# Optimization experiments

Hardware: AMD Instinct MI355X
Metric: run time of the kernel (lower is better)

## Reference

```python
import jax, jax.numpy as jnp
import numpy as np

B, T, F, H = 256, 100, 256, 512
EPS = 1e-9


def _uni(k, shape, fan):
    s = 1.0 / np.sqrt(fan)
    return jax.random.uniform(k, shape, jnp.float32, -s, s)


def setup_inputs() -> dict:
    key = jax.random.key(0)
    ks = jax.random.split(key, 20)
    values = jax.random.normal(ks[0], (B, T, F), jnp.float32)
    masks = (jax.random.uniform(ks[1], (B, T, F)) > 0.2).astype(jnp.float32)
    deltas = jax.random.uniform(ks[2], (B, T, F), jnp.float32) * 5.0
    return {
        "values": values, "masks": masks, "deltas": deltas,
        # TemporalDecay h: W [H,F], stdv=1/sqrt(H)
        "W_td_h": _uni(ks[3], (H, F), H), "b_td_h": _uni(ks[4], (H,), H),
        # TemporalDecay x (diag): W [F,F], stdv=1/sqrt(F)
        "W_td_x": _uni(ks[5], (F, F), F), "b_td_x": _uni(ks[6], (F,), F),
        # hist_reg Linear(H->F): stdv=1/sqrt(H)
        "W_hist": _uni(ks[7], (F, H), H), "b_hist": _uni(ks[8], (F,), H),
        "W_feat": _uni(ks[9], (F, F), F), "b_feat": _uni(ks[10], (F,), F),
        # combining_weight Linear(2F->F): stdv=1/sqrt(2F)
        "W_comb": _uni(ks[11], (F, 2 * F), 2 * F), "b_comb": _uni(ks[12], (F,), 2 * F),
        # LSTMCell(2F -> H): stdv=1/sqrt(H)
        "W_ih": _uni(ks[13], (4 * H, 2 * F), H), "W_hh": _uni(ks[14], (4 * H, H), H),
        "b_ih": _uni(ks[15], (4 * H,), H), "b_hh": _uni(ks[16], (4 * H,), H),
    }


def _mae(pred, target, mask):
    return jnp.sum(jnp.abs(pred - target) * mask) / (jnp.sum(mask) + EPS)


def reference(values, masks, deltas, W_td_h, b_td_h, W_td_x, b_td_x,
              W_hist, b_hist, W_feat, b_feat, W_comb, b_comb,
              W_ih, W_hh, b_ih, b_hh):
    diag_td_x = jnp.diagonal(W_td_x)               # F.linear(d, W*eye) == d * diag(W)
    Wf_masked = W_feat * (1.0 - jnp.eye(F, dtype=W_feat.dtype))

    def step(carry, xs):
        h, c, loss = carry
        x, m, d = xs                               # [B,F] each
        gamma_h = jnp.exp(-jax.nn.relu(d @ W_td_h.T + b_td_h))   # [B,H]
        gamma_x = jnp.exp(-jax.nn.relu(d * diag_td_x + b_td_x))  # [B,F]
        h = h * gamma_h
        x_h = h @ W_hist.T + b_hist
        loss = loss + _mae(x_h, x, m)
        x_c = m * x + (1.0 - m) * x_h
        z_h = jax.nn.relu(x_c @ Wf_masked.T + b_feat)
        loss = loss + _mae(z_h, x, m)
        alpha = jax.nn.sigmoid(jnp.concatenate([gamma_x, m], axis=1) @ W_comb.T + b_comb)
        c_h = alpha * z_h + (1.0 - alpha) * x_h
        loss = loss + _mae(c_h, x, m)
        c_c = m * x + (1.0 - m) * c_h
        inp = jnp.concatenate([c_c, m], axis=1)    # [B,2F]
        gates = inp @ W_ih.T + b_ih + h @ W_hh.T + b_hh
        i_g, f_g, g_g, o_g = jnp.split(gates, 4, axis=1)
        c = jax.nn.sigmoid(f_g) * c + jax.nn.sigmoid(i_g) * jnp.tanh(g_g)
        h = jax.nn.sigmoid(o_g) * jnp.tanh(c)
        return (h, c, loss), c_h

    h0 = jnp.zeros((values.shape[0], H), values.dtype)
    c0 = jnp.zeros((values.shape[0], H), values.dtype)
    xs = (jnp.swapaxes(values, 0, 1), jnp.swapaxes(masks, 0, 1), jnp.swapaxes(deltas, 0, 1))
    (h, c, loss), ests = jax.lax.scan(step, (h0, c0, jnp.float32(0.0)), xs)
    estimations = jnp.swapaxes(ests, 0, 1)         # [B,T,F]
    imputed = masks * values + (1.0 - masks) * estimations
    recon_loss = loss / (T * 3)
    return imputed, h, recon_loss
```

## Files before the change

### kernel.cpp

```cpp
#include <hip/hip_runtime.h>
#include <math.h>


#define T_ 100

typedef unsigned short ushortT;
typedef __attribute__((ext_vector_type(8))) short short8;
typedef __attribute__((ext_vector_type(4))) float f32x4;

#define OB_HD0    1048576u
#define OB_HD1    1310720u
#define OB_XCB    1835008u
#define OB_CCB    1966080u
#define OB_NUM2   2097152u
#define OB_DEN    2122752u
#define OB_CNT    2123264u
#define OB_BIASP  2123776u
#define OB_BA     2131968u
#define OB_BB     2394112u
#define OB_BC     2525184u
#define OB_MT     6719488u
#define OB_GH     19826688u
#define OB_AL     46041088u
#define OB_FLG1   59148288u
#define OB_FLG2   59152384u

__device__ __forceinline__ float sigm(float x) { return 1.0f / (1.0f + expf(-x)); }

__device__ __forceinline__ ushortT f2bf(float f) {
    union { float f; unsigned u; } v; v.f = f;
    unsigned r = v.u + 0x7fffu + ((v.u >> 16) & 1u);
    return (ushortT)(r >> 16);
}
__device__ __forceinline__ float bf2f(ushortT h) {
    union { unsigned u; float f; } v; v.u = ((unsigned)h) << 16; return v.f;
}

__device__ __forceinline__ void st_bf16_wt(ushortT* p, ushortT v) {
    asm volatile("global_store_short %0, %1, off sc0 sc1" :: "v"(p), "v"((unsigned)v) : "memory");
}
__device__ __forceinline__ void st_f32_wt(float* p, float v) {
    asm volatile("global_store_dword %0, %1, off sc0 sc1" :: "v"(p), "v"(v) : "memory");
}
__device__ __forceinline__ void st_u32_wt(unsigned* p, unsigned v) {
    asm volatile("global_store_dword %0, %1, off sc0 sc1" :: "v"(p), "v"(v) : "memory");
}

__device__ __forceinline__ void gbar(unsigned* cnt, unsigned* flags, unsigned epoch,
                                     unsigned nwg, unsigned myid, unsigned* rel) {
    asm volatile("s_waitcnt vmcnt(0)" ::: "memory");
    __syncthreads();
    if (threadIdx.x == 0) {
        unsigned old = __hip_atomic_fetch_add(cnt, 1u, __ATOMIC_RELAXED, __HIP_MEMORY_SCOPE_AGENT);
        *rel = (old == epoch * nwg - 1u) ? 1u : 0u;
    }
    __syncthreads();
    if (*rel) {
        if (threadIdx.x < nwg) st_u32_wt(&flags[threadIdx.x * 16], epoch);
    } else if (threadIdx.x == 0) {
        while (__hip_atomic_load(&flags[myid * 16], __ATOMIC_RELAXED, __HIP_MEMORY_SCOPE_AGENT) < epoch)
            __builtin_amdgcn_s_sleep(8);
    }
    if (threadIdx.x == 0)
        __builtin_amdgcn_fence(__ATOMIC_ACQUIRE, "agent");
    __syncthreads();
}


__global__ __launch_bounds__(256) void k_init2(unsigned char* wsb) {
    unsigned i = blockIdx.x * 256u + threadIdx.x;
    unsigned* w = (unsigned*)wsb;
    if (i < 327680u) w[i] = 0u;
    else if (i < 332800u) ((unsigned*)(wsb + OB_FLG1))[i - 327680u] = 0u;
    if (i == 0) {
        *(unsigned*)(wsb + OB_CNT) = 0u;
        *(unsigned*)(wsb + OB_CNT + 128) = 0u;
    }
}

__global__ __launch_bounds__(256) void k_prep2(const float* __restrict__ W_ih,
                                               const float* __restrict__ W_hh,
                                               const float* __restrict__ b_ih,
                                               const float* __restrict__ b_hh,
                                               const float* __restrict__ W_hist,
                                               const float* __restrict__ W_feat,
                                               unsigned char* wsb) {
    ushortT* Bc = (ushortT*)(wsb + OB_BC);
    ushortT* Ba = (ushortT*)(wsb + OB_BA);
    ushortT* Bb = (ushortT*)(wsb + OB_BB);
    float* biasp = (float*)(wsb + OB_BIASP);
    int n = blockIdx.x;
    int j = n >> 2, g = n & 3;
    int src = g * 512 + j;
    for (int k = threadIdx.x; k < 512; k += 256) {
        Bc[(size_t)n * 1024 + k]       = f2bf(W_ih[(size_t)src * 512 + k]);
        Bc[(size_t)n * 1024 + 512 + k] = f2bf(W_hh[(size_t)src * 512 + k]);
        if (n < 256) {
            Ba[(size_t)n * 512 + k] = f2bf(W_hist[(size_t)n * 512 + k]);
            if (k < 256) Bb[(size_t)n * 256 + k] = (k == n) ? 0 : f2bf(W_feat[(size_t)n * 256 + k]);
        }
    }
    if (threadIdx.x == 0) biasp[n] = b_ih[src] + b_hh[src];
}

__global__ __launch_bounds__(256) void k_den(const float* __restrict__ masks, unsigned char* wsb) {
    __shared__ float red[256];
    float* den = (float*)(wsb + OB_DEN);
    int t = blockIdx.x;
    float s = 0.0f;
    for (int idx = threadIdx.x; idx < 256 * 256; idx += 256) {
        int b = idx >> 8, f = idx & 255;
        s += masks[((size_t)b * T_ + t) * 256 + f];
    }
    red[threadIdx.x] = s; __syncthreads();
    for (int st = 128; st > 0; st >>= 1) { if (threadIdx.x < st) red[threadIdx.x] += red[threadIdx.x + st]; __syncthreads(); }
    if (threadIdx.x == 0) den[t] = red[0];
}

__global__ __launch_bounds__(256) void k_maskt(const float* __restrict__ masks, unsigned char* wsb) {
    ushortT* mt = (ushortT*)(wsb + OB_MT);
    unsigned gidx = blockIdx.x * 256u + threadIdx.x;
    int f4 = gidx & 63;
    unsigned rest = gidx >> 6;
    int t = rest % 100, b = rest / 100;
    float4 m = *(const float4*)(masks + ((size_t)b * T_ + t) * 256 + f4 * 4);
    size_t o = ((size_t)t * 256 + b) * 256 + f4 * 4;
    mt[o + 0] = f2bf(m.x); mt[o + 1] = f2bf(m.y); mt[o + 2] = f2bf(m.z); mt[o + 3] = f2bf(m.w);
}

__global__ __launch_bounds__(256) void k_gamma_h(const float* __restrict__ deltas,
                                                 const float* __restrict__ W,
                                                 const float* __restrict__ bias,
                                                 unsigned char* wsb) {
    ushortT* gh = (ushortT*)(wsb + OB_GH);
    __shared__ float As[16][65];
    __shared__ float Bs[16][65];
    int tid = threadIdx.x;
    int tx = tid & 15, ty = tid >> 4;
    int mb = blockIdx.x * 64, nb = blockIdx.y * 64;
    int lr = tid >> 2, lk = (tid & 3) * 4;
    float acc[4][4] = {};
    for (int k0 = 0; k0 < 256; k0 += 16) {
        float4 a = *(const float4*)(deltas + (size_t)(mb + lr) * 256 + k0 + lk);
        float4 b = *(const float4*)(W + (size_t)(nb + lr) * 256 + k0 + lk);
        As[lk + 0][lr] = a.x; As[lk + 1][lr] = a.y; As[lk + 2][lr] = a.z; As[lk + 3][lr] = a.w;
        Bs[lk + 0][lr] = b.x; Bs[lk + 1][lr] = b.y; Bs[lk + 2][lr] = b.z; Bs[lk + 3][lr] = b.w;
        __syncthreads();
#pragma unroll
        for (int kk = 0; kk < 16; kk++) {
            float av[4], bv[4];
#pragma unroll
            for (int i = 0; i < 4; i++) av[i] = As[kk][ty * 4 + i];
#pragma unroll
            for (int j = 0; j < 4; j++) bv[j] = Bs[kk][tx * 4 + j];
#pragma unroll
            for (int i = 0; i < 4; i++)
#pragma unroll
                for (int j = 0; j < 4; j++) acc[i][j] = fmaf(av[i], bv[j], acc[i][j]);
        }
        __syncthreads();
    }
#pragma unroll
    for (int i = 0; i < 4; i++) {
        int r = mb + ty * 4 + i;
#pragma unroll
        for (int j = 0; j < 4; j++) {
            int n = nb + tx * 4 + j;
            float v = acc[i][j] + bias[n];
            gh[(size_t)r * 512 + n] = f2bf(expf(-fmaxf(v, 0.0f)));
        }
    }
}

__global__ __launch_bounds__(256) void k_alpha(const float* __restrict__ deltas,
                                               const float* __restrict__ masks,
                                               const float* __restrict__ Wtdx,
                                               const float* __restrict__ btdx,
                                               const float* __restrict__ Wc,
                                               const float* __restrict__ bc,
                                               unsigned char* wsb) {
    ushortT* al = (ushortT*)(wsb + OB_AL);
    __shared__ float As[16][65];
    __shared__ float Bs[16][65];
    int tid = threadIdx.x;
    int tx = tid & 15, ty = tid >> 4;
    int mb = blockIdx.x * 64, nb = blockIdx.y * 64;
    int lr = tid >> 2, lk = (tid & 3) * 4;
    float acc[4][4] = {};
    for (int k0 = 0; k0 < 512; k0 += 16) {
        int kg = k0 + lk;
        float4 a;
        if (kg < 256) {
            float4 d4 = *(const float4*)(deltas + (size_t)(mb + lr) * 256 + kg);
            a.x = expf(-fmaxf(d4.x * Wtdx[(size_t)(kg + 0) * 257] + btdx[kg + 0], 0.0f));
            a.y = expf(-fmaxf(d4.y * Wtdx[(size_t)(kg + 1) * 257] + btdx[kg + 1], 0.0f));
            a.z = expf(-fmaxf(d4.z * Wtdx[(size_t)(kg + 2) * 257] + btdx[kg + 2], 0.0f));
            a.w = expf(-fmaxf(d4.w * Wtdx[(size_t)(kg + 3) * 257] + btdx[kg + 3], 0.0f));
        } else {
            a = *(const float4*)(masks + (size_t)(mb + lr) * 256 + (kg - 256));
        }
        float4 b = *(const float4*)(Wc + (size_t)(nb + lr) * 512 + kg);
        As[lk + 0][lr] = a.x; As[lk + 1][lr] = a.y; As[lk + 2][lr] = a.z; As[lk + 3][lr] = a.w;
        Bs[lk + 0][lr] = b.x; Bs[lk + 1][lr] = b.y; Bs[lk + 2][lr] = b.z; Bs[lk + 3][lr] = b.w;
        __syncthreads();
#pragma unroll
        for (int kk = 0; kk < 16; kk++) {
            float av[4], bv[4];
#pragma unroll
            for (int i = 0; i < 4; i++) av[i] = As[kk][ty * 4 + i];
#pragma unroll
            for (int j = 0; j < 4; j++) bv[j] = Bs[kk][tx * 4 + j];
#pragma unroll
            for (int i = 0; i < 4; i++)
#pragma unroll
                for (int j = 0; j < 4; j++) acc[i][j] = fmaf(av[i], bv[j], acc[i][j]);
        }
        __syncthreads();
    }
#pragma unroll
    for (int i = 0; i < 4; i++) {
        int r = mb + ty * 4 + i;
#pragma unroll
        for (int j = 0; j < 4; j++) {
            int n = nb + tx * 4 + j;
            al[(size_t)r * 256 + n] = f2bf(sigm(acc[i][j] + bc[n]));
        }
    }
}


__global__ __launch_bounds__(256, 1) void k_persist(const float* __restrict__ values,
                                                    const float* __restrict__ masks,
                                                    const float* __restrict__ b_hist,
                                                    const float* __restrict__ b_feat,
                                                    float* __restrict__ out,
                                                    unsigned char* __restrict__ wsb) {
    ushortT* hd[2] = { (ushortT*)(wsb + OB_HD0), (ushortT*)(wsb + OB_HD1) };
    ushortT* xcb = (ushortT*)(wsb + OB_XCB);
    ushortT* ccb = (ushortT*)(wsb + OB_CCB);
    float* num2 = (float*)(wsb + OB_NUM2);
    const float* den = (const float*)(wsb + OB_DEN);
    unsigned* cnt2 = (unsigned*)(wsb + OB_CNT);
    unsigned* cnt1 = (unsigned*)(wsb + OB_CNT + 128);
    unsigned* flg1 = (unsigned*)(wsb + OB_FLG1);
    unsigned* flg2 = (unsigned*)(wsb + OB_FLG2);
    const float* biasp = (const float*)(wsb + OB_BIASP);
    const ushortT* Ba = (const ushortT*)(wsb + OB_BA);
    const ushortT* Bb = (const ushortT*)(wsb + OB_BB);
    const ushortT* Bc = (const ushortT*)(wsb + OB_BC);
    const ushortT* mt = (const ushortT*)(wsb + OB_MT);
    const ushortT* gh = (const ushortT*)(wsb + OB_GH);
    const ushortT* al = (const ushortT*)(wsb + OB_AL);

    __shared__ ushortT ldsBc[32 * 1032];
    __shared__ ushortT ldsBa[16 * 520];
    __shared__ ushortT ldsBb[16 * 264];
    __shared__ float scr[4 * 16 * 36];
    __shared__ float lossSlots[8];
    __shared__ unsigned relsh;

    const int wg = blockIdx.x, tid = threadIdx.x;
    const int wave = tid >> 6, lane = tid & 63, quad = lane >> 4, l16 = lane & 15;

    {
        int n0 = (wg & 63) * 32;
        for (int i = tid; i < 4096; i += 256) {
            int r = i >> 7, c = i & 127;
            *(short8*)&ldsBc[r * 1032 + c * 8] = *(const short8*)&Bc[(size_t)(n0 + r) * 1024 + c * 8];
        }
        if (wg < 64) {
            int nA = (wg & 15) * 16;
            for (int i = tid; i < 1024; i += 256) {
                int r = i >> 6, c = i & 63;
                *(short8*)&ldsBa[r * 520 + c * 8] = *(const short8*)&Ba[(size_t)(nA + r) * 512 + c * 8];
            }
            for (int i = tid; i < 512; i += 256) {
                int r = i >> 5, c = i & 31;
                *(short8*)&ldsBb[r * 264 + c * 8] = *(const short8*)&Bb[(size_t)(nA + r) * 256 + c * 8];
            }
        }
        __syncthreads();
    }

    const int rgC = wg >> 6, cgC = wg & 63;
    const int r0C = rgC * 64 + wave * 16;
    const int n0C = cgC * 32;
    const float bp0 = biasp[n0C + l16];
    const float bp1 = biasp[n0C + 16 + l16];
    const int rowl = lane >> 2, q4 = lane & 3;
    const int bbE = rgC * 64 + wave * 16 + rowl;
    const int j0E = cgC * 8 + q4, j1E = j0E + 4;
    float creg0 = 0.f, creg1 = 0.f;

#pragma unroll 1
    for (int t = 0; t < T_; ++t) {
        const ushortT* hdA = hd[t & 1];
        ushortT* hdW = hd[(t + 1) & 1];

        if (wg < 64) {
            int mb = (wg >> 4) * 64, nb = (wg & 15) * 16;
            int rowA = mb + wave * 16;
            int n = nb + l16;
            float xhv[4];

            {
                f32x4 acc = {0.f, 0.f, 0.f, 0.f};
                const ushortT* aBase = hdA + (size_t)(rowA + l16) * 512 + quad * 8;
#pragma unroll 8
                for (int kc = 0; kc < 16; ++kc) {
                    short8 a = *(const short8*)(aBase + kc * 32);
                    short8 b = *(const short8*)&ldsBa[l16 * 520 + kc * 32 + quad * 8];
                    acc = __builtin_amdgcn_mfma_f32_16x16x32_bf16(a, b, acc, 0, 0, 0);
                }
                float bh = b_hist[n];
                float ls = 0.f;
#pragma unroll
                for (int r4 = 0; r4 < 4; ++r4) {
                    int r = rowA + quad * 4 + r4;
                    float v = acc[r4] + bh;
                    xhv[r4] = v;
                    size_t idx = ((size_t)r * T_ + t) * 256 + n;
                    float x = values[idx], m = masks[idx];
                    st_bf16_wt(&xcb[r * 256 + n], f2bf(m * x + (1.f - m) * v));
                    ls += fabsf(v - x) * m;
                }
                for (int off = 32; off; off >>= 1) ls += __shfl_down(ls, off);
                if (lane == 0) lossSlots[wave] = ls;
            }
            gbar(cnt1, flg1, (unsigned)(t + 1), 64u, (unsigned)wg, &relsh);

            {
                f32x4 acc = {0.f, 0.f, 0.f, 0.f};
                const ushortT* aBase = xcb + (size_t)(rowA + l16) * 256 + quad * 8;
#pragma unroll
                for (int kc = 0; kc < 8; ++kc) {
                    short8 a = *(const short8*)(aBase + kc * 32);
                    short8 b = *(const short8*)&ldsBb[l16 * 264 + kc * 32 + quad * 8];
                    acc = __builtin_amdgcn_mfma_f32_16x16x32_bf16(a, b, acc, 0, 0, 0);
                }
                float bfv = b_feat[n];
                float ls = 0.f;
#pragma unroll
                for (int r4 = 0; r4 < 4; ++r4) {
                    int r = rowA + quad * 4 + r4;
                    float z = fmaxf(acc[r4] + bfv, 0.f);
                    size_t idx = ((size_t)r * T_ + t) * 256 + n;
                    float a_ = bf2f(al[idx]);
                    float ch = a_ * z + (1.f - a_) * xhv[r4];
                    float x = values[idx], m = masks[idx];
                    float ccv = m * x + (1.f - m) * ch;
                    out[idx] = ccv;
                    st_bf16_wt(&ccb[r * 256 + n], f2bf(ccv));
                    ls += (fabsf(z - x) + fabsf(ch - x)) * m;
                }
                for (int off = 32; off; off >>= 1) ls += __shfl_down(ls, off);
                if (lane == 0) lossSlots[4 + wave] = ls;
                __syncthreads();
                if (tid == 0) {
                    float s = 0.f;
                    for (int i = 0; i < 8; ++i) s += lossSlots[i];
                    st_f32_wt(&num2[t * 64 + wg], s);
                }
            }
        }
        gbar(cnt2, flg2, (unsigned)(2 * t + 1), 256u, (unsigned)wg, &relsh);

        {
            f32x4 acc0 = {0.f, 0.f, 0.f, 0.f}, acc1 = {0.f, 0.f, 0.f, 0.f};
            const int lb0 = l16 * 1032 + quad * 8;
            const int lb1 = (16 + l16) * 1032 + quad * 8;
            {
                const ushortT* ap = ccb + (size_t)(r0C + l16) * 256 + quad * 8;
#pragma unroll
                for (int kc = 0; kc < 8; ++kc) {
                    short8 a  = *(const short8*)(ap + kc * 32);
                    short8 b0 = *(const short8*)&ldsBc[lb0 + kc * 32];
                    short8 b1 = *(const short8*)&ldsBc[lb1 + kc * 32];
                    acc0 = __builtin_amdgcn_mfma_f32_16x16x32_bf16(a, b0, acc0, 0, 0, 0);
                    acc1 = __builtin_amdgcn_mfma_f32_16x16x32_bf16(a, b1, acc1, 0, 0, 0);
                }
            }
            {
                const ushortT* ap = mt + (size_t)t * 65536 + (size_t)(r0C + l16) * 256 + quad * 8;
#pragma unroll
                for (int kc = 0; kc < 8; ++kc) {
                    short8 a  = *(const short8*)(ap + kc * 32);
                    short8 b0 = *(const short8*)&ldsBc[lb0 + 256 + kc * 32];
                    short8 b1 = *(const short8*)&ldsBc[lb1 + 256 + kc * 32];
                    acc0 = __builtin_amdgcn_mfma_f32_16x16x32_bf16(a, b0, acc0, 0, 0, 0);
                    acc1 = __builtin_amdgcn_mfma_f32_16x16x32_bf16(a, b1, acc1, 0, 0, 0);
                }
            }
            {
                const ushortT* ap = hdA + (size_t)(r0C + l16) * 512 + quad * 8;
#pragma unroll 8
                for (int kc = 0; kc < 16; ++kc) {
                    short8 a  = *(const short8*)(ap + kc * 32);
                    short8 b0 = *(const short8*)&ldsBc[lb0 + 512 + kc * 32];
                    short8 b1 = *(const short8*)&ldsBc[lb1 + 512 + kc * 32];
                    acc0 = __builtin_amdgcn_mfma_f32_16x16x32_bf16(a, b0, acc0, 0, 0, 0);
                    acc1 = __builtin_amdgcn_mfma_f32_16x16x32_bf16(a, b1, acc1, 0, 0, 0);
                }
            }

            float* ms = scr + wave * (16 * 36);
#pragma unroll
            for (int r4 = 0; r4 < 4; ++r4) {
                ms[(quad * 4 + r4) * 36 + l16]      = acc0[r4] + bp0;
                ms[(quad * 4 + r4) * 36 + 16 + l16] = acc1[r4] + bp1;
            }
            const float* g0 = &ms[rowl * 36 + q4 * 4];
            const float* g1 = &ms[rowl * 36 + 16 + q4 * 4];
            float cn0 = sigm(g0[1]) * creg0 + sigm(g0[0]) * tanhf(g0[2]);
            float hn0 = sigm(g0[3]) * tanhf(cn0);
            float cn1 = sigm(g1[1]) * creg1 + sigm(g1[0]) * tanhf(g1[2]);
            float hn1 = sigm(g1[3]) * tanhf(cn1);
            creg0 = cn0; creg1 = cn1;
            if (t < T_ - 1) {
                float gv0 = bf2f(gh[((size_t)bbE * T_ + t + 1) * 512 + j0E]);
                float gv1 = bf2f(gh[((size_t)bbE * T_ + t + 1) * 512 + j1E]);
                st_bf16_wt(&hdW[(size_t)bbE * 512 + j0E], f2bf(hn0 * gv0));
                st_bf16_wt(&hdW[(size_t)bbE * 512 + j1E], f2bf(hn1 * gv1));
            } else {
                out[6553600 + (size_t)bbE * 512 + j0E] = hn0;
                out[6553600 + (size_t)bbE * 512 + j1E] = hn1;
            }
        }
        gbar(cnt2, flg2, (unsigned)(2 * t + 2), 256u, (unsigned)wg, &relsh);
    }

    if (wg == 0) {
        float v = 0.f;
        if (tid < T_) {
            float s = 0.f;
            for (int w = 0; w < 64; ++w) s += num2[tid * 64 + w];
            v = s / (den[tid] + 1e-9f);
        }
        scr[tid] = v;
        __syncthreads();
        for (int s = 128; s > 0; s >>= 1) { if (tid < s) scr[tid] += scr[tid + s]; __syncthreads(); }
        if (tid == 0) out[6684672] = scr[0] / 300.0f;
    }
}

extern "C" void kernel_launch(void* const* d_in, const int* in_sizes, int n_in,
                              void* d_out, int out_size, void* d_ws, size_t ws_size,
                              hipStream_t stream) {
    (void)in_sizes; (void)n_in; (void)out_size; (void)ws_size;
    const float* values = (const float*)d_in[0];
    const float* masks  = (const float*)d_in[1];
    const float* deltas = (const float*)d_in[2];
    const float* W_td_h = (const float*)d_in[3];
    const float* b_td_h = (const float*)d_in[4];
    const float* W_td_x = (const float*)d_in[5];
    const float* b_td_x = (const float*)d_in[6];
    const float* W_hist = (const float*)d_in[7];
    const float* b_hist = (const float*)d_in[8];
    const float* W_feat = (const float*)d_in[9];
    const float* b_feat = (const float*)d_in[10];
    const float* W_comb = (const float*)d_in[11];
    const float* b_comb = (const float*)d_in[12];
    const float* W_ih   = (const float*)d_in[13];
    const float* W_hh   = (const float*)d_in[14];
    const float* b_ih   = (const float*)d_in[15];
    const float* b_hh   = (const float*)d_in[16];

    unsigned char* wsb = (unsigned char*)d_ws;
    float* out = (float*)d_out;

    k_init2<<<1300, 256, 0, stream>>>(wsb);
    k_prep2<<<2048, 256, 0, stream>>>(W_ih, W_hh, b_ih, b_hh, W_hist, W_feat, wsb);
    k_den<<<100, 256, 0, stream>>>(masks, wsb);
    k_maskt<<<6400, 256, 0, stream>>>(masks, wsb);
    k_gamma_h<<<dim3(400, 8), 256, 0, stream>>>(deltas, W_td_h, b_td_h, wsb);
    k_alpha<<<dim3(400, 4), 256, 0, stream>>>(deltas, masks, W_td_x, b_td_x, W_comb, b_comb, wsb);
    k_persist<<<256, 256, 0, stream>>>(values, masks, b_hist, b_feat, out, wsb);
}
```

Baseline: 2.865 ms.

## Replace global barriers with per-batch-slice flag dataflow sync and overlap LSTM GEMM

Swaps the three grid-wide counter barriers per timestep for per-workgroup epoch flags grouped by batch slice (d = wg&3). Each consumer polls only the 16 or 64 producer flags it depends on. The LSTM gate GEMM parts that do not depend on the current step (mask and h parts) now run before waiting on the c_c producers, overlapping them with the x_h/z_h stages. The risks are subtle memory-ordering or race bugs from the relaxed flag protocol, and more polling traffic from many waiters.

After: 2.619 ms. 8.6% less time.

```diff
diff --git a/kernel.cpp b/kernel.cpp
--- a/kernel.cpp
+++ b/kernel.cpp
@@ -14,7 +14,6 @@
 #define OB_CCB    1966080u
 #define OB_NUM2   2097152u
 #define OB_DEN    2122752u
-#define OB_CNT    2123264u
 #define OB_BIASP  2123776u
 #define OB_BA     2131968u
 #define OB_BB     2394112u
@@ -22,8 +21,7 @@
 #define OB_MT     6719488u
 #define OB_GH     19826688u
 #define OB_AL     46041088u
-#define OB_FLG1   59148288u
-#define OB_FLG2   59152384u
+#define OB_FLG    59148288u
 
 __device__ __forceinline__ float sigm(float x) { return 1.0f / (1.0f + expf(-x)); }
 
@@ -46,36 +44,32 @@
     asm volatile("global_store_dword %0, %1, off sc0 sc1" :: "v"(p), "v"(v) : "memory");
 }
 
-__device__ __forceinline__ void gbar(unsigned* cnt, unsigned* flags, unsigned epoch,
-                                     unsigned nwg, unsigned myid, unsigned* rel) {
+__device__ __forceinline__ void bar_arrive(unsigned* slot, unsigned epoch) {
     asm volatile("s_waitcnt vmcnt(0)" ::: "memory");
     __syncthreads();
-    if (threadIdx.x == 0) {
-        unsigned old = __hip_atomic_fetch_add(cnt, 1u, __ATOMIC_RELAXED, __HIP_MEMORY_SCOPE_AGENT);
-        *rel = (old == epoch * nwg - 1u) ? 1u : 0u;
-    }
-    __syncthreads();
-    if (*rel) {
-        if (threadIdx.x < nwg) st_u32_wt(&flags[threadIdx.x * 16], epoch);
-    } else if (threadIdx.x == 0) {
-        while (__hip_atomic_load(&flags[myid * 16], __ATOMIC_RELAXED, __HIP_MEMORY_SCOPE_AGENT) < epoch)
-            __builtin_amdgcn_s_sleep(8);
-    }
-    if (threadIdx.x == 0)
-        __builtin_amdgcn_fence(__ATOMIC_ACQUIRE, "agent");
+    if (threadIdx.x == 0) st_u32_wt(slot, epoch);
+}
+
+__device__ __forceinline__ void bar_wait(const unsigned* flags, unsigned nf, unsigned epoch) {
+    if (threadIdx.x < 64) {
+        for (;;) {
+            unsigned f = epoch;
+            if (threadIdx.x < nf)
+                f = __hip_atomic_load(flags + threadIdx.x, __ATOMIC_RELAXED, __HIP_MEMORY_SCOPE_AGENT);
+            if (__all((int)(f >= epoch))) break;
+            __builtin_amdgcn_s_sleep(2);
+        }
+        if (threadIdx.x == 0)
+            __builtin_amdgcn_fence(__ATOMIC_ACQUIRE, "agent");
+    }
     __syncthreads();
 }
 
 
 __global__ __launch_bounds__(256) void k_init2(unsigned char* wsb) {
     unsigned i = blockIdx.x * 256u + threadIdx.x;
-    unsigned* w = (unsigned*)wsb;
-    if (i < 327680u) w[i] = 0u;
-    else if (i < 332800u) ((unsigned*)(wsb + OB_FLG1))[i - 327680u] = 0u;
-    if (i == 0) {
-        *(unsigned*)(wsb + OB_CNT) = 0u;
-        *(unsigned*)(wsb + OB_CNT + 128) = 0u;
-    }
+    if (i < 65536u) ((unsigned*)(wsb + OB_HD0))[i] = 0u;
+    if (i < 1024u)  ((unsigned*)(wsb + OB_FLG))[i] = 0u;
 }
 
 __global__ __launch_bounds__(256) void k_prep2(const float* __restrict__ W_ih,
@@ -240,10 +234,6 @@
     ushortT* ccb = (ushortT*)(wsb + OB_CCB);
     float* num2 = (float*)(wsb + OB_NUM2);
     const float* den = (const float*)(wsb + OB_DEN);
-    unsigned* cnt2 = (unsigned*)(wsb + OB_CNT);
-    unsigned* cnt1 = (unsigned*)(wsb + OB_CNT + 128);
-    unsigned* flg1 = (unsigned*)(wsb + OB_FLG1);
-    unsigned* flg2 = (unsigned*)(wsb + OB_FLG2);
     const float* biasp = (const float*)(wsb + OB_BIASP);
     const ushortT* Ba = (const ushortT*)(wsb + OB_BA);
     const ushortT* Bb = (const ushortT*)(wsb + OB_BB);
@@ -257,19 +247,26 @@
     __shared__ ushortT ldsBb[16 * 264];
     __shared__ float scr[4 * 16 * 36];
     __shared__ float lossSlots[8];
-    __shared__ unsigned relsh;
 
     const int wg = blockIdx.x, tid = threadIdx.x;
     const int wave = tid >> 6, lane = tid & 63, quad = lane >> 4, l16 = lane & 15;
+    const int d = wg & 3;
+    const int k = wg >> 2;
+
+    unsigned* flgs = (unsigned*)(wsb + OB_FLG);
+    unsigned* fA = flgs + d * 64;
+    unsigned* fB = flgs + 256 + d * 64;
+    unsigned* fC = flgs + 512 + d * 64;
+    unsigned* cntF = flgs + 768;
 
     {
-        int n0 = (wg & 63) * 32;
+        int n0 = k * 32;
         for (int i = tid; i < 4096; i += 256) {
             int r = i >> 7, c = i & 127;
             *(short8*)&ldsBc[r * 1032 + c * 8] = *(const short8*)&Bc[(size_t)(n0 + r) * 1024 + c * 8];
         }
         if (wg < 64) {
-            int nA = (wg & 15) * 16;
+            int nA = k * 16;
             for (int i = tid; i < 1024; i += 256) {
                 int r = i >> 6, c = i & 63;
                 *(short8*)&ldsBa[r * 520 + c * 8] = *(const short8*)&Ba[(size_t)(nA + r) * 512 + c * 8];
@@ -282,127 +279,126 @@
         __syncthreads();
     }
 
-    const int rgC = wg >> 6, cgC = wg & 63;
-    const int r0C = rgC * 64 + wave * 16;
-    const int n0C = cgC * 32;
-    const float bp0 = biasp[n0C + l16];
-    const float bp1 = biasp[n0C + 16 + l16];
+    const int r0C = d * 64 + wave * 16;
+    const int lb0 = l16 * 1032 + quad * 8;
+    const int lb1 = (16 + l16) * 1032 + quad * 8;
+    const float bp0 = biasp[k * 32 + l16];
+    const float bp1 = biasp[k * 32 + 16 + l16];
     const int rowl = lane >> 2, q4 = lane & 3;
-    const int bbE = rgC * 64 + wave * 16 + rowl;
-    const int j0E = cgC * 8 + q4, j1E = j0E + 4;
+    const int bbE = r0C + rowl;
+    const int j0E = k * 8 + q4, j1E = j0E + 4;
     float creg0 = 0.f, creg1 = 0.f;
+
+    const int nbA = k * 16;
+    const int nA_ = nbA + l16;
 
 #pragma unroll 1
     for (int t = 0; t < T_; ++t) {
         const ushortT* hdA = hd[t & 1];
         ushortT* hdW = hd[(t + 1) & 1];
 
+        if (t) bar_wait(fC, 64, (unsigned)t);
+
+        float xhv[4], xr[4], mr[4];
+
         if (wg < 64) {
-            int mb = (wg >> 4) * 64, nb = (wg & 15) * 16;
-            int rowA = mb + wave * 16;
-            int n = nb + l16;
-            float xhv[4];
-
-            {
-                f32x4 acc = {0.f, 0.f, 0.f, 0.f};
-                const ushortT* aBase = hdA + (size_t)(rowA + l16) * 512 + quad * 8;
+            f32x4 acc = {0.f, 0.f, 0.f, 0.f};
+            const ushortT* aBase = hdA + (size_t)(r0C + l16) * 512 + quad * 8;
 #pragma unroll 8
-                for (int kc = 0; kc < 16; ++kc) {
-                    short8 a = *(const short8*)(aBase + kc * 32);
-                    short8 b = *(const short8*)&ldsBa[l16 * 520 + kc * 32 + quad * 8];
-                    acc = __builtin_amdgcn_mfma_f32_16x16x32_bf16(a, b, acc, 0, 0, 0);
-                }
-                float bh = b_hist[n];
-                float ls = 0.f;
-#pragma unroll
-                for (int r4 = 0; r4 < 4; ++r4) {
-                    int r = rowA + quad * 4 + r4;
-                    float v = acc[r4] + bh;
-                    xhv[r4] = v;
-                    size_t idx = ((size_t)r * T_ + t) * 256 + n;
-                    float x = values[idx], m = masks[idx];
-                    st_bf16_wt(&xcb[r * 256 + n], f2bf(m * x + (1.f - m) * v));
-                    ls += fabsf(v - x) * m;
-                }
-                for (int off = 32; off; off >>= 1) ls += __shfl_down(ls, off);
-                if (lane == 0) lossSlots[wave] = ls;
-            }
-            gbar(cnt1, flg1, (unsigned)(t + 1), 64u, (unsigned)wg, &relsh);
-
-            {
-                f32x4 acc = {0.f, 0.f, 0.f, 0.f};
-                const ushortT* aBase = xcb + (size_t)(rowA + l16) * 256 + quad * 8;
-#pragma unroll
-                for (int kc = 0; kc < 8; ++kc) {
-                    short8 a = *(const short8*)(aBase + kc * 32);
-                    short8 b = *(const short8*)&ldsBb[l16 * 264 + kc * 32 + quad * 8];
-                    acc = __builtin_amdgcn_mfma_f32_16x16x32_bf16(a, b, acc, 0, 0, 0);
-                }
-                float bfv = b_feat[n];
-                float ls = 0.f;
-#pragma unroll
-                for (int r4 = 0; r4 < 4; ++r4) {
-                    int r = rowA + quad * 4 + r4;
-                    float z = fmaxf(acc[r4] + bfv, 0.f);
-                    size_t idx = ((size_t)r * T_ + t) * 256 + n;
-                    float a_ = bf2f(al[idx]);
-                    float ch = a_ * z + (1.f - a_) * xhv[r4];
-                    float x = values[idx], m = masks[idx];
-                    float ccv = m * x + (1.f - m) * ch;
-                    out[idx] = ccv;
-                    st_bf16_wt(&ccb[r * 256 + n], f2bf(ccv));
-                    ls += (fabsf(z - x) + fabsf(ch - x)) * m;
-                }
-                for (int off = 32; off; off >>= 1) ls += __shfl_down(ls, off);
-                if (lane == 0) lossSlots[4 + wave] = ls;
-                __syncthreads();
-                if (tid == 0) {
-                    float s = 0.f;
-                    for (int i = 0; i < 8; ++i) s += lossSlots[i];
-                    st_f32_wt(&num2[t * 64 + wg], s);
-                }
-            }
-        }
-        gbar(cnt2, flg2, (unsigned)(2 * t + 1), 256u, (unsigned)wg, &relsh);
-
+            for (int kc = 0; kc < 16; ++kc) {
+                short8 a = *(const short8*)(aBase + kc * 32);
+                short8 b = *(const short8*)&ldsBa[l16 * 520 + kc * 32 + quad * 8];
+                acc = __builtin_amdgcn_mfma_f32_16x16x32_bf16(a, b, acc, 0, 0, 0);
+            }
+            float bh = b_hist[nA_];
+            float ls = 0.f;
+#pragma unroll
+            for (int r4 = 0; r4 < 4; ++r4) {
+                int r = r0C + quad * 4 + r4;
+                float v = acc[r4] + bh;
+                xhv[r4] = v;
+                size_t idx = ((size_t)r * T_ + t) * 256 + nA_;
+                xr[r4] = values[idx]; mr[r4] = masks[idx];
+                st_bf16_wt(&xcb[r * 256 + nA_], f2bf(mr[r4] * xr[r4] + (1.f - mr[r4]) * v));
+                ls += fabsf(v - xr[r4]) * mr[r4];
+            }
+            for (int off = 32; off; off >>= 1) ls += __shfl_down(ls, off);
+            if (lane == 0) lossSlots[wave] = ls;
+            bar_arrive(&fA[k], (unsigned)(t + 1));
+        }
+
+        f32x4 acc0 = {0.f, 0.f, 0.f, 0.f}, acc1 = {0.f, 0.f, 0.f, 0.f};
         {
-            f32x4 acc0 = {0.f, 0.f, 0.f, 0.f}, acc1 = {0.f, 0.f, 0.f, 0.f};
-            const int lb0 = l16 * 1032 + quad * 8;
-            const int lb1 = (16 + l16) * 1032 + quad * 8;
-            {
-                const ushortT* ap = ccb + (size_t)(r0C + l16) * 256 + quad * 8;
-#pragma unroll
-                for (int kc = 0; kc < 8; ++kc) {
-                    short8 a  = *(const short8*)(ap + kc * 32);
-                    short8 b0 = *(const short8*)&ldsBc[lb0 + kc * 32];
-                    short8 b1 = *(const short8*)&ldsBc[lb1 + kc * 32];
-                    acc0 = __builtin_amdgcn_mfma_f32_16x16x32_bf16(a, b0, acc0, 0, 0, 0);
-                    acc1 = __builtin_amdgcn_mfma_f32_16x16x32_bf16(a, b1, acc1, 0, 0, 0);
-                }
-            }
-            {
-                const ushortT* ap = mt + (size_t)t * 65536 + (size_t)(r0C + l16) * 256 + quad * 8;
-#pragma unroll
-                for (int kc = 0; kc < 8; ++kc) {
-                    short8 a  = *(const short8*)(ap + kc * 32);
-                    short8 b0 = *(const short8*)&ldsBc[lb0 + 256 + kc * 32];
-                    short8 b1 = *(const short8*)&ldsBc[lb1 + 256 + kc * 32];
-                    acc0 = __builtin_amdgcn_mfma_f32_16x16x32_bf16(a, b0, acc0, 0, 0, 0);
-                    acc1 = __builtin_amdgcn_mfma_f32_16x16x32_bf16(a, b1, acc1, 0, 0, 0);
-                }
-            }
-            {
-                const ushortT* ap = hdA + (size_t)(r0C + l16) * 512 + quad * 8;
+            const ushortT* ap = mt + (size_t)t * 65536 + (size_t)(r0C + l16) * 256 + quad * 8;
+#pragma unroll
+            for (int kc = 0; kc < 8; ++kc) {
+                short8 a  = *(const short8*)(ap + kc * 32);
+                short8 b0 = *(const short8*)&ldsBc[lb0 + 256 + kc * 32];
+                short8 b1 = *(const short8*)&ldsBc[lb1 + 256 + kc * 32];
+                acc0 = __builtin_amdgcn_mfma_f32_16x16x32_bf16(a, b0, acc0, 0, 0, 0);
+                acc1 = __builtin_amdgcn_mfma_f32_16x16x32_bf16(a, b1, acc1, 0, 0, 0);
+            }
+        }
+        {
+            const ushortT* ap = hdA + (size_t)(r0C + l16) * 512 + quad * 8;
 #pragma unroll 8
-                for (int kc = 0; kc < 16; ++kc) {
-                    short8 a  = *(const short8*)(ap + kc * 32);
-                    short8 b0 = *(const short8*)&ldsBc[lb0 + 512 + kc * 32];
-                    short8 b1 = *(const short8*)&ldsBc[lb1 + 512 + kc * 32];
-                    acc0 = __builtin_amdgcn_mfma_f32_16x16x32_bf16(a, b0, acc0, 0, 0, 0);
-                    acc1 = __builtin_amdgcn_mfma_f32_16x16x32_bf16(a, b1, acc1, 0, 0, 0);
-                }
-            }
-
+            for (int kc = 0; kc < 16; ++kc) {
+                short8 a  = *(const short8*)(ap + kc * 32);
+                short8 b0 = *(const short8*)&ldsBc[lb0 + 512 + kc * 32];
+                short8 b1 = *(const short8*)&ldsBc[lb1 + 512 + kc * 32];
+                acc0 = __builtin_amdgcn_mfma_f32_16x16x32_bf16(a, b0, acc0, 0, 0, 0);
+                acc1 = __builtin_amdgcn_mfma_f32_16x16x32_bf16(a, b1, acc1, 0, 0, 0);
+            }
+        }
+
+        if (wg < 64) {
+            bar_wait(fA, 16, (unsigned)(t + 1));
+            f32x4 acc = {0.f, 0.f, 0.f, 0.f};
+            const ushortT* aBase = xcb + (size_t)(r0C + l16) * 256 + quad * 8;
+#pragma unroll
+            for (int kc = 0; kc < 8; ++kc) {
+                short8 a = *(const short8*)(aBase + kc * 32);
+                short8 b = *(const short8*)&ldsBb[l16 * 264 + kc * 32 + quad * 8];
+                acc = __builtin_amdgcn_mfma_f32_16x16x32_bf16(a, b, acc, 0, 0, 0);
+            }
+            float bfv = b_feat[nA_];
+            float ls = 0.f;
+#pragma unroll
+            for (int r4 = 0; r4 < 4; ++r4) {
+                int r = r0C + quad * 4 + r4;
+                float z = fmaxf(acc[r4] + bfv, 0.f);
+                size_t idx = ((size_t)r * T_ + t) * 256 + nA_;
+                float a_ = bf2f(al[idx]);
+                float ch = a_ * z + (1.f - a_) * xhv[r4];
+                float ccv = mr[r4] * xr[r4] + (1.f - mr[r4]) * ch;
+                out[idx] = ccv;
+                st_bf16_wt(&ccb[r * 256 + nA_], f2bf(ccv));
+                ls += (fabsf(z - xr[r4]) + fabsf(ch - xr[r4])) * mr[r4];
+            }
+            for (int off = 32; off; off >>= 1) ls += __shfl_down(ls, off);
+            if (lane == 0) lossSlots[4 + wave] = ls;
+            __syncthreads();
+            if (tid == 0) {
+                float s = 0.f;
+                for (int i = 0; i < 8; ++i) s += lossSlots[i];
+                st_f32_wt(&num2[t * 64 + wg], s);
+            }
+            bar_arrive(&fB[k], (unsigned)(t + 1));
+        }
+
+        bar_wait(fB, 16, (unsigned)(t + 1));
+        {
+            const ushortT* ap = ccb + (size_t)(r0C + l16) * 256 + quad * 8;
+#pragma unroll
+            for (int kc = 0; kc < 8; ++kc) {
+                short8 a  = *(const short8*)(ap + kc * 32);
+                short8 b0 = *(const short8*)&ldsBc[lb0 + kc * 32];
+                short8 b1 = *(const short8*)&ldsBc[lb1 + kc * 32];
+                acc0 = __builtin_amdgcn_mfma_f32_16x16x32_bf16(a, b0, acc0, 0, 0, 0);
+                acc1 = __builtin_amdgcn_mfma_f32_16x16x32_bf16(a, b1, acc1, 0, 0, 0);
+            }
+        }
+        {
             float* ms = scr + wave * (16 * 36);
 #pragma unroll
             for (int r4 = 0; r4 < 4; ++r4) {
@@ -421,15 +417,23 @@
                 float gv1 = bf2f(gh[((size_t)bbE * T_ + t + 1) * 512 + j1E]);
                 st_bf16_wt(&hdW[(size_t)bbE * 512 + j0E], f2bf(hn0 * gv0));
                 st_bf16_wt(&hdW[(size_t)bbE * 512 + j1E], f2bf(hn1 * gv1));
+                bar_arrive(&fC[k], (unsigned)(t + 1));
             } else {
                 out[6553600 + (size_t)bbE * 512 + j0E] = hn0;
                 out[6553600 + (size_t)bbE * 512 + j1E] = hn1;
             }
         }
-        gbar(cnt2, flg2, (unsigned)(2 * t + 2), 256u, (unsigned)wg, &relsh);
-    }
-
+    }
+
+    if (tid == 0)
+        __hip_atomic_fetch_add(cntF, 1u, __ATOMIC_RELAXED, __HIP_MEMORY_SCOPE_AGENT);
     if (wg == 0) {
+        if (tid == 0) {
+            while (__hip_atomic_load(cntF, __ATOMIC_RELAXED, __HIP_MEMORY_SCOPE_AGENT) < 256u)
+                __builtin_amdgcn_s_sleep(2);
+            __builtin_amdgcn_fence(__ATOMIC_ACQUIRE, "agent");
+        }
+        __syncthreads();
         float v = 0.f;
         if (tid < T_) {
             float s = 0.f;
@@ -468,7 +472,7 @@
     unsigned char* wsb = (unsigned char*)d_ws;
     float* out = (float*)d_out;
 
-    k_init2<<<1300, 256, 0, stream>>>(wsb);
+    k_init2<<<256, 256, 0, stream>>>(wsb);
     k_prep2<<<2048, 256, 0, stream>>>(W_ih, W_hh, b_ih, b_hh, W_hist, W_feat, wsb);
     k_den<<<100, 256, 0, stream>>>(masks, wsb);
     k_maskt<<<6400, 256, 0, stream>>>(masks, wsb);
```
